# Kernel tuning notes

Measured on AMD Instinct MI355X. Metric: run time of the kernel, lower is better.

## Reference

```python
import jax, jax.numpy as jnp
import numpy as np

C_IN = 128
C_HID = 32
N_HEADS = 4
INF = 1000000000.0


def setup_inputs() -> dict:
    key = jax.random.key(0)
    ks = jax.random.split(key, 12)
    B, I, J = 1, 256, 256
    hc = N_HEADS * C_HID
    s = 0.02
    return {
        "x": jax.random.normal(ks[0], (B, I, J, C_IN), dtype=jnp.float32),
        "mask": jnp.ones((B, I, J), dtype=jnp.float32),
        "ln_w": jnp.ones((C_IN,), dtype=jnp.float32),
        "ln_b": jnp.zeros((C_IN,), dtype=jnp.float32),
        "w_tri": jax.random.normal(ks[1], (C_IN, N_HEADS), dtype=jnp.float32) * s,
        "wq": jax.random.normal(ks[2], (C_IN, hc), dtype=jnp.float32) * s,
        "wk": jax.random.normal(ks[3], (C_IN, hc), dtype=jnp.float32) * s,
        "wv": jax.random.normal(ks[4], (C_IN, hc), dtype=jnp.float32) * s,
        "wg": jax.random.normal(ks[5], (C_IN, hc), dtype=jnp.float32) * s,
        "bg": jnp.ones((hc,), dtype=jnp.float32),
        "wo": jax.random.normal(ks[6], (hc, C_IN), dtype=jnp.float32) * s,
        "bo": jnp.zeros((C_IN,), dtype=jnp.float32),
    }


def _layer_norm(x, w, b, eps=1e-5):
    mu = jnp.mean(x, axis=-1, keepdims=True)
    var = jnp.var(x, axis=-1, keepdims=True)
    return (x - mu) * jax.lax.rsqrt(var + eps) * w + b


def _triangle_attention(x, mask, ln_w, ln_b, w_tri, wq, wk, wv, wg, bg, wo, bo):
    # starting=True: no transpose. x: [B, I, J, C]
    B, I, J, C = x.shape
    x = _layer_norm(x, ln_w, ln_b)
    # mask_bias: [B, I, 1, 1, J]
    mask_bias = (INF * (mask - 1.0))[..., :, None, None, :]
    # triangle_bias: linear(x) -> [B, I, J, H], permute (2,0,1) -> [B, H, I, J], unsqueeze -> [B, 1, H, I, J]
    tri = jnp.einsum("bijc,ch->bhij", x, w_tri)[:, None]  # [B, 1, H, I, J]
    # q/k/v: [B, I, H, J, Ch]
    def proj(w):
        return jnp.einsum("bijc,c(" + "" + ")->bijc", x, w) if False else (
            (x @ w).reshape(B, I, J, N_HEADS, C_HID).transpose(0, 1, 3, 2, 4))
    q = proj(wq) * (C_HID ** -0.5)
    k = proj(wk)
    v = proj(wv)
    # scores: [B, I, H, J, J]; biases broadcast over H (mask_bias) / I (tri over b,1 dim matches i? no)
    scores = jnp.einsum("bihqc,bihkc->bihqk", q, k)
    scores = scores + mask_bias + tri  # tri [B,1,H,I,J] broadcasts: i-dim aligns with query? matches torch broadcast [B,I,H,J,J]+[B,1,H,J,J]... wait tri is [B,1,H,I,J] with I==J so it broadcasts over the batch-of-rows dim
    a = jax.nn.softmax(scores, axis=-1)
    o = jnp.einsum("bihqk,bihkc->bihqc", a, v)  # [B, I, H, J, Ch]
    o = o.transpose(0, 1, 3, 2, 4).reshape(B, I, J, N_HEADS * C_HID)
    g = jax.nn.sigmoid(x @ wg + bg)
    o = o * g
    return o @ wo + bo  # [B, I, J, C]


def reference(x, mask, ln_w, ln_b, w_tri, wq, wk, wv, wg, bg, wo, bo):
    return _triangle_attention(x, mask, ln_w, ln_b, w_tri, wq, wk, wv, wg, bg, wo, bo)
```

## Files before the change

kernel.cpp:

```cpp
#include <hip/hip_runtime.h>


typedef __attribute__((ext_vector_type(4))) float f32x4;
typedef __attribute__((ext_vector_type(8))) short bf16x8;
#define MFMA16(a, b, c) __builtin_amdgcn_mfma_f32_16x16x32_bf16(a, b, c, 0, 0, 0)
#define LOG2E 1.4426950408889634f

__device__ __forceinline__ float bf2f(unsigned int u16) {
    return __uint_as_float(u16 << 16);
}
__device__ __forceinline__ unsigned int f2bf(float f) {
    unsigned int u = __float_as_uint(f);
    return (u + 0x7fffu + ((u >> 16) & 1u)) >> 16;
}
__device__ __forceinline__ unsigned int pack2(float a, float b) {
    return f2bf(a) | (f2bf(b) << 16);
}
__device__ __forceinline__ unsigned int cvt_pk_bf16(float lo, float hi) {
    unsigned int r;
    asm("v_cvt_pk_bf16_f32 %0, %1, %2" : "=v"(r) : "v"(lo), "v"(hi));
    return r;
}

__global__ __launch_bounds__(128) void k_prep(
    const float* __restrict__ wq, const float* __restrict__ wk,
    const float* __restrict__ wv, const float* __restrict__ wg,
    const float* __restrict__ wo, unsigned short* __restrict__ wT)
{
    const int mat = blockIdx.x, k0 = blockIdx.y * 16, t = threadIdx.x;
    const float* W = (mat == 0) ? wq : (mat == 1) ? wk : (mat == 2) ? wv
                     : (mat == 3) ? wg : wo;
    unsigned short* T = wT + mat * 16384;
    float col[16];
    #pragma unroll
    for (int kk = 0; kk < 16; ++kk) col[kk] = W[(k0 + kk) * 128 + t];
    unsigned int pk[8];
    #pragma unroll
    for (int u = 0; u < 8; ++u) pk[u] = pack2(col[2 * u], col[2 * u + 1]);
    *(uint4*)(T + t * 128 + k0)     = make_uint4(pk[0], pk[1], pk[2], pk[3]);
    *(uint4*)(T + t * 128 + k0 + 8) = make_uint4(pk[4], pk[5], pk[6], pk[7]);
}

__global__ __launch_bounds__(256, 2) void k_lnproj(
    const float* __restrict__ x, const float* __restrict__ ln_w,
    const float* __restrict__ ln_b, const float* __restrict__ w_tri,
    const unsigned short* __restrict__ wT, const float* __restrict__ bg,
    unsigned short* __restrict__ qb, unsigned short* __restrict__ kb,
    unsigned short* __restrict__ vtb, unsigned short* __restrict__ gb,
    float* __restrict__ triT)
{
    __shared__ unsigned short sA[128 * 136];
    __shared__ unsigned short sB[128 * 136];
    __shared__ unsigned short sWt[16 * 136];

    const int t = threadIdx.x, w = t >> 6, lane = t & 63;
    const int l15 = lane & 15, g = lane >> 4;
    const int rowBase = blockIdx.x * 128;

    if (t < 128) {
        const float4 wv = ((const float4*)w_tri)[t];
        sWt[0 * 136 + t] = (unsigned short)f2bf(wv.x);
        sWt[1 * 136 + t] = (unsigned short)f2bf(wv.y);
        sWt[2 * 136 + t] = (unsigned short)f2bf(wv.z);
        sWt[3 * 136 + t] = (unsigned short)f2bf(wv.w);
    } else {
        #pragma unroll
        for (int u = 0; u < 13; ++u) {
            const int idx = (t - 128) + 128 * u;
            if (idx < 12 * 136) sWt[4 * 136 + idx] = 0;
        }
    }

    {
        const int r = t >> 1, half = t & 1;
        const float* xr = x + (size_t)(rowBase + r) * 128 + half * 64;
        float v[64];
        float s1 = 0.0f, s2 = 0.0f;
        #pragma unroll
        for (int u = 0; u < 16; ++u) {
            const float4 q4 = ((const float4*)xr)[u];
            v[4*u] = q4.x; v[4*u+1] = q4.y; v[4*u+2] = q4.z; v[4*u+3] = q4.w;
            s1 += q4.x + q4.y + q4.z + q4.w;
            s2 += q4.x*q4.x + q4.y*q4.y + q4.z*q4.z + q4.w*q4.w;
        }
        s1 += __shfl_xor(s1, 1);
        s2 += __shfl_xor(s2, 1);
        const float mu = s1 * (1.0f / 128.0f);
        const float rs = rsqrtf(s2 * (1.0f / 128.0f) - mu * mu + 1e-5f);
        const float4* lw = (const float4*)(ln_w + half * 64);
        const float4* lb = (const float4*)(ln_b + half * 64);
        #pragma unroll
        for (int u = 0; u < 16; ++u) {
            const float4 w4 = lw[u], b4 = lb[u];
            v[4*u]   = (v[4*u]   - mu) * rs * w4.x + b4.x;
            v[4*u+1] = (v[4*u+1] - mu) * rs * w4.y + b4.y;
            v[4*u+2] = (v[4*u+2] - mu) * rs * w4.z + b4.z;
            v[4*u+3] = (v[4*u+3] - mu) * rs * w4.w + b4.w;
        }
        #pragma unroll
        for (int u = 0; u < 8; ++u) {
            uint4 pk;
            pk.x = pack2(v[8*u],   v[8*u+1]);
            pk.y = pack2(v[8*u+2], v[8*u+3]);
            pk.z = pack2(v[8*u+4], v[8*u+5]);
            pk.w = pack2(v[8*u+6], v[8*u+7]);
            *(uint4*)&sA[r * 136 + half * 64 + u * 8] = pk;
        }
    }
    __syncthreads();

    bf16x8 af[2][4];
    #pragma unroll
    for (int m = 0; m < 2; ++m)
        #pragma unroll
        for (int ks = 0; ks < 4; ++ks)
            af[m][ks] = *(const bf16x8*)&sA[(w * 32 + m * 16 + l15) * 136 + ks * 32 + g * 8];

    #pragma unroll
    for (int m = 0; m < 2; ++m) {
        f32x4 tc = (f32x4){0.f, 0.f, 0.f, 0.f};
        #pragma unroll
        for (int ks = 0; ks < 4; ++ks) {
            const bf16x8 bfw = *(const bf16x8*)&sWt[l15 * 136 + ks * 32 + g * 8];
            tc = MFMA16(af[m][ks], bfw, tc);
        }
        if (l15 < 4) {
            #pragma unroll
            for (int reg = 0; reg < 4; ++reg) {
                const int gr = rowBase + w * 32 + m * 16 + 4 * g + reg;
                triT[l15 * 65536 + gr] = tc[reg] * LOG2E;
            }
        }
    }

    const int r2 = t >> 1, half2 = t & 1;
    for (int mat = 0; mat < 4; ++mat) {
        {
            const unsigned short* Wm = wT + mat * 16384 + r2 * 128 + half2 * 64;
            #pragma unroll
            for (int u = 0; u < 8; ++u)
                *(uint4*)&sB[r2 * 136 + half2 * 64 + u * 8] = *(const uint4*)(Wm + u * 8);
        }
        __syncthreads();

        f32x4 acc[2][8];
        #pragma unroll
        for (int m = 0; m < 2; ++m)
            #pragma unroll
            for (int n = 0; n < 8; ++n) acc[m][n] = (f32x4){0.f, 0.f, 0.f, 0.f};
        #pragma unroll
        for (int n = 0; n < 8; ++n)
            #pragma unroll
            for (int ks = 0; ks < 4; ++ks) {
                const bf16x8 bf = *(const bf16x8*)&sB[(n * 16 + l15) * 136 + ks * 32 + g * 8];
                acc[0][n] = MFMA16(af[0][ks], bf, acc[0][n]);
                acc[1][n] = MFMA16(af[1][ks], bf, acc[1][n]);
            }
        __syncthreads();

        float bgv[8];
        if (mat == 3) {
            #pragma unroll
            for (int n = 0; n < 8; ++n) bgv[n] = bg[n * 16 + l15];
        }
        const float scl = (mat == 0) ? 0.25503486245f : 1.0f;
        #pragma unroll
        for (int m = 0; m < 2; ++m)
            #pragma unroll
            for (int n = 0; n < 8; ++n) {
                float vv[4];
                #pragma unroll
                for (int reg = 0; reg < 4; ++reg) {
                    float z = acc[m][n][reg];
                    if (mat == 3) z = 1.0f / (1.0f + __expf(-(z + bgv[n])));
                    else z *= scl;
                    vv[reg] = z;
                }
                const unsigned int a01 = cvt_pk_bf16(vv[0], vv[1]);
                const unsigned int a23 = cvt_pk_bf16(vv[2], vv[3]);
                const int qr = w * 32 + m * 16 + g * 4;
                const int col = n * 16 + l15;
                sB[qr * 136 + col]       = (unsigned short)a01;
                sB[(qr + 1) * 136 + col] = (unsigned short)(a01 >> 16);
                sB[(qr + 2) * 136 + col] = (unsigned short)a23;
                sB[(qr + 3) * 136 + col] = (unsigned short)(a23 >> 16);
            }
        __syncthreads();

        const int row = rowBase + r2;
        if (mat < 2) {
            unsigned short* dst = (mat == 0) ? qb : kb;
            const int i = row >> 8, j = row & 255;
            #pragma unroll
            for (int u = 0; u < 8; ++u) {
                const int c0 = half2 * 64 + u * 8;
                const int hh = c0 >> 5, ch = c0 & 31;
                *(uint4*)(dst + (((size_t)(i * 4 + hh)) * 256 + j) * 32 + ch) =
                    *(const uint4*)&sB[r2 * 136 + c0];
            }
        } else if (mat == 2) {
            const int c = t & 127, jh = t >> 7;
            const int i = rowBase >> 8;
            const int j0 = (rowBase & 255) + jh * 64;
            unsigned short buf[64];
            #pragma unroll
            for (int u = 0; u < 64; ++u) buf[u] = sB[(jh * 64 + u) * 136 + c];
            unsigned short* dst = vtb + ((size_t)(i * 128 + c)) * 256 + j0;
            #pragma unroll
            for (int u = 0; u < 8; ++u)
                *(uint4*)(dst + u * 8) = *(uint4*)&buf[u * 8];
        } else {
            #pragma unroll
            for (int u = 0; u < 8; ++u) {
                const int c0 = half2 * 64 + u * 8;
                *(uint4*)(gb + (size_t)row * 128 + c0) = *(const uint4*)&sB[r2 * 136 + c0];
            }
        }
        __syncthreads();
    }
}

__global__ __launch_bounds__(256, 3) void k_attn5(
    const unsigned short* __restrict__ qb, const unsigned short* __restrict__ kb,
    const unsigned short* __restrict__ vtb, const float* __restrict__ mask,
    const float* __restrict__ triT, unsigned short* __restrict__ ob)
{
    __shared__ unsigned short sK[256 * 36];
    __shared__ unsigned short sP[4][64 * 64];
    __shared__ float sM[256];

    const int i = blockIdx.x, h = blockIdx.y, t = threadIdx.x;
    const int w = t >> 6, lane = t & 63, l15 = lane & 15, g = lane >> 4;
    const size_t base = (size_t)(i * 4 + h) * 8192;

    {
        const uint4* ks = (const uint4*)(kb + base + t * 32);
        uint4 k0 = ks[0], k1 = ks[1], k2 = ks[2], k3 = ks[3];
        *(uint4*)&sK[t * 36]      = k0;
        *(uint4*)&sK[t * 36 + 8]  = k1;
        *(uint4*)&sK[t * 36 + 16] = k2;
        *(uint4*)&sK[t * 36 + 24] = k3;
        sM[t] = (LOG2E * 1.0e9f) * (mask[i * 256 + t] - 1.0f);
    }

    const int q0 = w * 64;
    bf16x8 qf[4];
    #pragma unroll
    for (int m = 0; m < 4; ++m)
        qf[m] = *(const bf16x8*)(qb + base + (size_t)(q0 + m * 16 + l15) * 32 + g * 8);

    bf16x8 ones;
    #pragma unroll
    for (int u = 0; u < 8; ++u) ones[u] = (short)0x3F80;

    __syncthreads();

    f32x4 acc[4][2], accL[4];
    #pragma unroll
    for (int m = 0; m < 4; ++m) {
        acc[m][0] = (f32x4){0.f, 0.f, 0.f, 0.f};
        acc[m][1] = (f32x4){0.f, 0.f, 0.f, 0.f};
        accL[m]   = (f32x4){0.f, 0.f, 0.f, 0.f};
    }

    char* sPw = (char*)&sP[w][0];
    const int swz = (l15 & 7) << 4;
    const float* triQ = triT + h * 65536;
    const f32x4 zero = (f32x4){0.f, 0.f, 0.f, 0.f};

    for (int kt = 0; kt < 4; ++kt) {
        const int kv0 = kt * 64;
        bf16x8 kf[4];
        #pragma unroll
        for (int n = 0; n < 4; ++n)
            kf[n] = *(const bf16x8*)&sK[(kv0 + n * 16 + l15) * 36 + g * 8];

        float4 mk[4];
        #pragma unroll
        for (int n = 0; n < 4; ++n) mk[n] = *(const float4*)&sM[kv0 + n * 16 + g * 4];

        float4 tvb[2][4];
        #pragma unroll
        for (int n = 0; n < 4; ++n)
            tvb[0][n] = *(const float4*)(triQ + (q0 + l15) * 256 + kv0 + n * 16 + g * 4);

        #pragma unroll
        for (int m = 0; m < 4; ++m) {
            f32x4 p[4];
            #pragma unroll
            for (int n = 0; n < 4; ++n)
                p[n] = MFMA16(kf[n], qf[m], zero);
            if (m < 3) {
                #pragma unroll
                for (int n = 0; n < 4; ++n)
                    tvb[(m + 1) & 1][n] = *(const float4*)
                        (triQ + (q0 + (m + 1) * 16 + l15) * 256 + kv0 + n * 16 + g * 4);
            }
            #pragma unroll
            for (int n = 0; n < 4; ++n) {
                const float4 tv = tvb[m & 1][n];
                p[n][0] = exp2f(p[n][0] + mk[n].x + tv.x);
                p[n][1] = exp2f(p[n][1] + mk[n].y + tv.y);
                p[n][2] = exp2f(p[n][2] + mk[n].z + tv.z);
                p[n][3] = exp2f(p[n][3] + mk[n].w + tv.w);
            }
            #pragma unroll
            for (int n = 0; n < 4; ++n) {
                const unsigned int a01 = cvt_pk_bf16(p[n][0], p[n][1]);
                const unsigned int a23 = cvt_pk_bf16(p[n][2], p[n][3]);
                *(uint2*)(sPw + (m * 16 + l15) * 128 + ((n * 32 + g * 8) ^ swz)) =
                    make_uint2(a01, a23);
            }
        }

        #pragma unroll
        for (int ks = 0; ks < 2; ++ks) {
            const bf16x8 vf0 = *(const bf16x8*)
                (vtb + base + (size_t)l15 * 256 + kv0 + ks * 32 + g * 8);
            const bf16x8 vf1 = *(const bf16x8*)
                (vtb + base + (size_t)(16 + l15) * 256 + kv0 + ks * 32 + g * 8);
            #pragma unroll
            for (int m = 0; m < 4; ++m) {
                const bf16x8 pb = *(const bf16x8*)
                    (sPw + (m * 16 + l15) * 128 + ((ks * 64 + g * 16) ^ swz));
                acc[m][0] = MFMA16(vf0, pb, acc[m][0]);
                acc[m][1] = MFMA16(vf1, pb, acc[m][1]);
                accL[m]   = MFMA16(ones, pb, accL[m]);
            }
        }
    }

    #pragma unroll
    for (int m = 0; m < 4; ++m) {
        const float inv = 1.0f / accL[m][0];
        const int q = q0 + m * 16 + l15;
        unsigned short* op = ob + (((size_t)(i * 256 + q)) * 4 + h) * 32;
        #pragma unroll
        for (int n2 = 0; n2 < 2; ++n2) {
            const unsigned int a01 = cvt_pk_bf16(acc[m][n2][0] * inv, acc[m][n2][1] * inv);
            const unsigned int a23 = cvt_pk_bf16(acc[m][n2][2] * inv, acc[m][n2][3] * inv);
            *(uint2*)(op + n2 * 16 + g * 4) = make_uint2(a01, a23);
        }
    }
}

__global__ __launch_bounds__(256, 2) void k_out2(
    const unsigned short* __restrict__ ob, const unsigned short* __restrict__ gb,
    const unsigned short* __restrict__ woT, const float* __restrict__ bo,
    float* __restrict__ out)
{
    __shared__ unsigned short sA[128 * 136];
    __shared__ unsigned short sB[128 * 136];
    const int t = threadIdx.x, w = t >> 6, lane = t & 63;
    const int l15 = lane & 15, g = lane >> 4;
    const int rowBase = blockIdx.x * 128;

    {
        const int r = t >> 1, half = t & 1;
        #pragma unroll
        for (int u = 0; u < 8; ++u) {
            const int c = half * 64 + u * 8;
            const uint4 ov = *(const uint4*)(ob + (size_t)(rowBase + r) * 128 + c);
            const uint4 gv = *(const uint4*)(gb + (size_t)(rowBase + r) * 128 + c);
            uint4 pr;
            pr.x = cvt_pk_bf16(bf2f(ov.x & 0xffffu) * bf2f(gv.x & 0xffffu),
                               bf2f(ov.x >> 16) * bf2f(gv.x >> 16));
            pr.y = cvt_pk_bf16(bf2f(ov.y & 0xffffu) * bf2f(gv.y & 0xffffu),
                               bf2f(ov.y >> 16) * bf2f(gv.y >> 16));
            pr.z = cvt_pk_bf16(bf2f(ov.z & 0xffffu) * bf2f(gv.z & 0xffffu),
                               bf2f(ov.z >> 16) * bf2f(gv.z >> 16));
            pr.w = cvt_pk_bf16(bf2f(ov.w & 0xffffu) * bf2f(gv.w & 0xffffu),
                               bf2f(ov.w >> 16) * bf2f(gv.w >> 16));
            *(uint4*)&sA[r * 136 + c] = pr;
            *(uint4*)&sB[r * 136 + c] = *(const uint4*)(woT + r * 128 + c);
        }
    }
    __syncthreads();

    f32x4 acc[2][8];
    #pragma unroll
    for (int m = 0; m < 2; ++m)
        #pragma unroll
        for (int n = 0; n < 8; ++n) acc[m][n] = (f32x4){0.f, 0.f, 0.f, 0.f};

    bf16x8 af[2][4];
    #pragma unroll
    for (int m = 0; m < 2; ++m)
        #pragma unroll
        for (int ks = 0; ks < 4; ++ks)
            af[m][ks] = *(const bf16x8*)&sA[(w * 32 + m * 16 + l15) * 136 + ks * 32 + g * 8];
    #pragma unroll
    for (int n = 0; n < 8; ++n) {
        #pragma unroll
        for (int ks = 0; ks < 4; ++ks) {
            const bf16x8 bf = *(const bf16x8*)&sB[(n * 16 + l15) * 136 + ks * 32 + g * 8];
            acc[0][n] = MFMA16(af[0][ks], bf, acc[0][n]);
            acc[1][n] = MFMA16(af[1][ks], bf, acc[1][n]);
        }
    }

    float bov[8];
    #pragma unroll
    for (int n = 0; n < 8; ++n) bov[n] = bo[n * 16 + l15];
    #pragma unroll
    for (int m = 0; m < 2; ++m)
        #pragma unroll
        for (int n = 0; n < 8; ++n)
            #pragma unroll
            for (int reg = 0; reg < 4; ++reg) {
                const int row = rowBase + w * 32 + m * 16 + g * 4 + reg;
                out[(size_t)row * 128 + n * 16 + l15] = acc[m][n][reg] + bov[n];
            }
}

extern "C" void kernel_launch(void* const* d_in, const int* in_sizes, int n_in,
                              void* d_out, int out_size, void* d_ws, size_t ws_size,
                              hipStream_t stream) {
    (void)in_sizes; (void)n_in; (void)out_size; (void)ws_size;
    const float* x     = (const float*)d_in[0];
    const float* mask  = (const float*)d_in[1];
    const float* ln_w  = (const float*)d_in[2];
    const float* ln_b  = (const float*)d_in[3];
    const float* w_tri = (const float*)d_in[4];
    const float* wq    = (const float*)d_in[5];
    const float* wk    = (const float*)d_in[6];
    const float* wv    = (const float*)d_in[7];
    const float* wg    = (const float*)d_in[8];
    const float* bg    = (const float*)d_in[9];
    const float* wo    = (const float*)d_in[10];
    const float* bo    = (const float*)d_in[11];
    float* out = (float*)d_out;

    char* ws = (char*)d_ws;
    unsigned short* qb   = (unsigned short*)(ws + (16u << 20));
    unsigned short* kb   = (unsigned short*)(ws + (32u << 20));
    unsigned short* vtb  = (unsigned short*)(ws + (48u << 20));
    unsigned short* gb   = (unsigned short*)(ws + (64u << 20));
    unsigned short* ob   = (unsigned short*)(ws + (80u << 20));
    float*          triT = (float*)(ws + (96u << 20));
    unsigned short* wT   = (unsigned short*)(ws + (97u << 20));

    k_prep<<<dim3(5, 8), 128, 0, stream>>>(wq, wk, wv, wg, wo, wT);
    k_lnproj<<<512, 256, 0, stream>>>(x, ln_w, ln_b, w_tri, wT, bg,
                                      qb, kb, vtb, gb, triT);
    k_attn5<<<dim3(256, 4), 256, 0, stream>>>(qb, kb, vtb, mask, triT, ob);
    k_out2<<<512, 256, 0, stream>>>(ob, gb, wT + 4 * 16384, bo, out);
}
```

Baseline: 123.3 us.

## Fuse gating into attention epilogue, stage V in LDS, shrink out-proj LDS

Moves the sigmoid-gate multiply from the output-projection kernel into the attention kernel epilogue, so the output kernel no longer reads the gate tensor. The attention kernel now stages V^T into shared memory, processes keys in 32-wide halves with a smaller P buffer, and uses an XOR swizzle for K in LDS. The output kernel loads the weight matrix in two K-chunks to cut LDS use and raise occupancy to three blocks per CU. The costs are extra barriers in the output kernel, more LDS in the attention kernel, and an extra gate read per attention block.

```diff
diff --git a/kernel.cpp b/kernel.cpp
--- a/kernel.cpp
+++ b/kernel.cpp
@@ -220,13 +220,15 @@
     }
 }
 
-__global__ __launch_bounds__(256, 3) void k_attn5(
+__global__ __launch_bounds__(256, 3) void k_attn6(
     const unsigned short* __restrict__ qb, const unsigned short* __restrict__ kb,
     const unsigned short* __restrict__ vtb, const float* __restrict__ mask,
-    const float* __restrict__ triT, unsigned short* __restrict__ ob)
+    const float* __restrict__ triT, const unsigned short* __restrict__ gb,
+    unsigned short* __restrict__ ob)
 {
-    __shared__ unsigned short sK[256 * 36];
-    __shared__ unsigned short sP[4][64 * 64];
+    __shared__ unsigned short sK[256 * 32];
+    __shared__ unsigned short sVt[32 * 260];
+    __shared__ unsigned short sP[4][64 * 36];
     __shared__ float sM[256];
 
     const int i = blockIdx.x, h = blockIdx.y, t = threadIdx.x;
@@ -235,11 +237,19 @@
 
     {
         const uint4* ks = (const uint4*)(kb + base + t * 32);
-        uint4 k0 = ks[0], k1 = ks[1], k2 = ks[2], k3 = ks[3];
-        *(uint4*)&sK[t * 36]      = k0;
-        *(uint4*)&sK[t * 36 + 8]  = k1;
-        *(uint4*)&sK[t * 36 + 16] = k2;
-        *(uint4*)&sK[t * 36 + 24] = k3;
+        char* kdst = (char*)sK + t * 64;
+        const int kswz = (t & 3) << 4;
+        #pragma unroll
+        for (int u = 0; u < 4; ++u)
+            *(uint4*)(kdst + ((u * 16) ^ kswz)) = ks[u];
+
+        const int ch = t >> 3, seg = t & 7;
+        const uint4* vs = (const uint4*)(vtb + base + (size_t)ch * 256 + seg * 32);
+        unsigned short* vdst = &sVt[ch * 260 + seg * 32];
+        #pragma unroll
+        for (int u = 0; u < 4; ++u)
+            *(uint4*)(vdst + u * 8) = vs[u];
+
         sM[t] = (LOG2E * 1.0e9f) * (mask[i * 256 + t] - 1.0f);
     }
 
@@ -263,66 +273,69 @@
         accL[m]   = (f32x4){0.f, 0.f, 0.f, 0.f};
     }
 
-    char* sPw = (char*)&sP[w][0];
-    const int swz = (l15 & 7) << 4;
+    unsigned short* sPw = &sP[w][0];
     const float* triQ = triT + h * 65536;
     const f32x4 zero = (f32x4){0.f, 0.f, 0.f, 0.f};
 
+    #pragma unroll
     for (int kt = 0; kt < 4; ++kt) {
         const int kv0 = kt * 64;
-        bf16x8 kf[4];
-        #pragma unroll
-        for (int n = 0; n < 4; ++n)
-            kf[n] = *(const bf16x8*)&sK[(kv0 + n * 16 + l15) * 36 + g * 8];
-
-        float4 mk[4];
-        #pragma unroll
-        for (int n = 0; n < 4; ++n) mk[n] = *(const float4*)&sM[kv0 + n * 16 + g * 4];
-
-        float4 tvb[2][4];
-        #pragma unroll
-        for (int n = 0; n < 4; ++n)
-            tvb[0][n] = *(const float4*)(triQ + (q0 + l15) * 256 + kv0 + n * 16 + g * 4);
-
-        #pragma unroll
-        for (int m = 0; m < 4; ++m) {
-            f32x4 p[4];
-            #pragma unroll
-            for (int n = 0; n < 4; ++n)
-                p[n] = MFMA16(kf[n], qf[m], zero);
-            if (m < 3) {
+        #pragma unroll
+        for (int hh = 0; hh < 2; ++hh) {
+            const int kvh = kv0 + hh * 32;
+
+            bf16x8 kf[2];
+            #pragma unroll
+            for (int n2 = 0; n2 < 2; ++n2) {
+                const int row = kvh + n2 * 16 + l15;
+                kf[n2] = *(const bf16x8*)((const char*)sK + row * 64 +
+                                          ((g * 16) ^ ((row & 3) << 4)));
+            }
+            float4 mk[2];
+            #pragma unroll
+            for (int n2 = 0; n2 < 2; ++n2)
+                mk[n2] = *(const float4*)&sM[kvh + n2 * 16 + g * 4];
+
+            float4 tvb[2][2];
+            #pragma unroll
+            for (int n2 = 0; n2 < 2; ++n2)
+                tvb[0][n2] = *(const float4*)
+                    (triQ + (q0 + l15) * 256 + kvh + n2 * 16 + g * 4);
+
+            #pragma unroll
+            for (int m = 0; m < 4; ++m) {
+                f32x4 p[2];
                 #pragma unroll
-                for (int n = 0; n < 4; ++n)
-                    tvb[(m + 1) & 1][n] = *(const float4*)
-                        (triQ + (q0 + (m + 1) * 16 + l15) * 256 + kv0 + n * 16 + g * 4);
-            }
-            #pragma unroll
-            for (int n = 0; n < 4; ++n) {
-                const float4 tv = tvb[m & 1][n];
-                p[n][0] = exp2f(p[n][0] + mk[n].x + tv.x);
-                p[n][1] = exp2f(p[n][1] + mk[n].y + tv.y);
-                p[n][2] = exp2f(p[n][2] + mk[n].z + tv.z);
-                p[n][3] = exp2f(p[n][3] + mk[n].w + tv.w);
-            }
-            #pragma unroll
-            for (int n = 0; n < 4; ++n) {
-                const unsigned int a01 = cvt_pk_bf16(p[n][0], p[n][1]);
-                const unsigned int a23 = cvt_pk_bf16(p[n][2], p[n][3]);
-                *(uint2*)(sPw + (m * 16 + l15) * 128 + ((n * 32 + g * 8) ^ swz)) =
-                    make_uint2(a01, a23);
-            }
-        }
-
-        #pragma unroll
-        for (int ks = 0; ks < 2; ++ks) {
-            const bf16x8 vf0 = *(const bf16x8*)
-                (vtb + base + (size_t)l15 * 256 + kv0 + ks * 32 + g * 8);
-            const bf16x8 vf1 = *(const bf16x8*)
-                (vtb + base + (size_t)(16 + l15) * 256 + kv0 + ks * 32 + g * 8);
+                for (int n2 = 0; n2 < 2; ++n2)
+                    p[n2] = MFMA16(kf[n2], qf[m], zero);
+                if (m < 3) {
+                    #pragma unroll
+                    for (int n2 = 0; n2 < 2; ++n2)
+                        tvb[(m + 1) & 1][n2] = *(const float4*)
+                            (triQ + (q0 + (m + 1) * 16 + l15) * 256 + kvh + n2 * 16 + g * 4);
+                }
+                #pragma unroll
+                for (int n2 = 0; n2 < 2; ++n2) {
+                    const float4 tv = tvb[m & 1][n2];
+                    p[n2][0] = exp2f(p[n2][0] + mk[n2].x + tv.x);
+                    p[n2][1] = exp2f(p[n2][1] + mk[n2].y + tv.y);
+                    p[n2][2] = exp2f(p[n2][2] + mk[n2].z + tv.z);
+                    p[n2][3] = exp2f(p[n2][3] + mk[n2].w + tv.w);
+                }
+                #pragma unroll
+                for (int n2 = 0; n2 < 2; ++n2) {
+                    const unsigned int a01 = cvt_pk_bf16(p[n2][0], p[n2][1]);
+                    const unsigned int a23 = cvt_pk_bf16(p[n2][2], p[n2][3]);
+                    *(uint2*)&sPw[(m * 16 + l15) * 36 + n2 * 16 + g * 4] =
+                        make_uint2(a01, a23);
+                }
+            }
+
+            const bf16x8 vf0 = *(const bf16x8*)&sVt[l15 * 260 + kvh + g * 8];
+            const bf16x8 vf1 = *(const bf16x8*)&sVt[(16 + l15) * 260 + kvh + g * 8];
             #pragma unroll
             for (int m = 0; m < 4; ++m) {
-                const bf16x8 pb = *(const bf16x8*)
-                    (sPw + (m * 16 + l15) * 128 + ((ks * 64 + g * 16) ^ swz));
+                const bf16x8 pb = *(const bf16x8*)&sPw[(m * 16 + l15) * 36 + g * 8];
                 acc[m][0] = MFMA16(vf0, pb, acc[m][0]);
                 acc[m][1] = MFMA16(vf1, pb, acc[m][1]);
                 accL[m]   = MFMA16(ones, pb, accL[m]);
@@ -334,48 +347,38 @@
     for (int m = 0; m < 4; ++m) {
         const float inv = 1.0f / accL[m][0];
         const int q = q0 + m * 16 + l15;
+        const unsigned short* gp = gb + (size_t)(i * 256 + q) * 128 + h * 32;
         unsigned short* op = ob + (((size_t)(i * 256 + q)) * 4 + h) * 32;
         #pragma unroll
         for (int n2 = 0; n2 < 2; ++n2) {
-            const unsigned int a01 = cvt_pk_bf16(acc[m][n2][0] * inv, acc[m][n2][1] * inv);
-            const unsigned int a23 = cvt_pk_bf16(acc[m][n2][2] * inv, acc[m][n2][3] * inv);
+            const uint2 gv = *(const uint2*)(gp + n2 * 16 + g * 4);
+            const float g0 = bf2f(gv.x & 0xffffu), g1 = bf2f(gv.x >> 16);
+            const float g2 = bf2f(gv.y & 0xffffu), g3 = bf2f(gv.y >> 16);
+            const unsigned int a01 =
+                cvt_pk_bf16(acc[m][n2][0] * inv * g0, acc[m][n2][1] * inv * g1);
+            const unsigned int a23 =
+                cvt_pk_bf16(acc[m][n2][2] * inv * g2, acc[m][n2][3] * inv * g3);
             *(uint2*)(op + n2 * 16 + g * 4) = make_uint2(a01, a23);
         }
     }
 }
 
-__global__ __launch_bounds__(256, 2) void k_out2(
-    const unsigned short* __restrict__ ob, const unsigned short* __restrict__ gb,
-    const unsigned short* __restrict__ woT, const float* __restrict__ bo,
-    float* __restrict__ out)
+__global__ __launch_bounds__(256, 3) void k_out3(
+    const unsigned short* __restrict__ ob, const unsigned short* __restrict__ woT,
+    const float* __restrict__ bo, float* __restrict__ out)
 {
     __shared__ unsigned short sA[128 * 136];
-    __shared__ unsigned short sB[128 * 136];
+    __shared__ unsigned short sB[128 * 72];
     const int t = threadIdx.x, w = t >> 6, lane = t & 63;
     const int l15 = lane & 15, g = lane >> 4;
     const int rowBase = blockIdx.x * 128;
-
-    {
-        const int r = t >> 1, half = t & 1;
-        #pragma unroll
-        for (int u = 0; u < 8; ++u) {
-            const int c = half * 64 + u * 8;
-            const uint4 ov = *(const uint4*)(ob + (size_t)(rowBase + r) * 128 + c);
-            const uint4 gv = *(const uint4*)(gb + (size_t)(rowBase + r) * 128 + c);
-            uint4 pr;
-            pr.x = cvt_pk_bf16(bf2f(ov.x & 0xffffu) * bf2f(gv.x & 0xffffu),
-                               bf2f(ov.x >> 16) * bf2f(gv.x >> 16));
-            pr.y = cvt_pk_bf16(bf2f(ov.y & 0xffffu) * bf2f(gv.y & 0xffffu),
-                               bf2f(ov.y >> 16) * bf2f(gv.y >> 16));
-            pr.z = cvt_pk_bf16(bf2f(ov.z & 0xffffu) * bf2f(gv.z & 0xffffu),
-                               bf2f(ov.z >> 16) * bf2f(gv.z >> 16));
-            pr.w = cvt_pk_bf16(bf2f(ov.w & 0xffffu) * bf2f(gv.w & 0xffffu),
-                               bf2f(ov.w >> 16) * bf2f(gv.w >> 16));
-            *(uint4*)&sA[r * 136 + c] = pr;
-            *(uint4*)&sB[r * 136 + c] = *(const uint4*)(woT + r * 128 + c);
-        }
-    }
-    __syncthreads();
+    const int r = t >> 1, half = t & 1;
+
+    #pragma unroll
+    for (int u = 0; u < 8; ++u) {
+        const int c = half * 64 + u * 8;
+        *(uint4*)&sA[r * 136 + c] = *(const uint4*)(ob + (size_t)(rowBase + r) * 128 + c);
+    }
 
     f32x4 acc[2][8];
     #pragma unroll
@@ -383,20 +386,27 @@
         #pragma unroll
         for (int n = 0; n < 8; ++n) acc[m][n] = (f32x4){0.f, 0.f, 0.f, 0.f};
 
-    bf16x8 af[2][4];
-    #pragma unroll
-    for (int m = 0; m < 2; ++m)
-        #pragma unroll
-        for (int ks = 0; ks < 4; ++ks)
-            af[m][ks] = *(const bf16x8*)&sA[(w * 32 + m * 16 + l15) * 136 + ks * 32 + g * 8];
-    #pragma unroll
-    for (int n = 0; n < 8; ++n) {
-        #pragma unroll
-        for (int ks = 0; ks < 4; ++ks) {
-            const bf16x8 bf = *(const bf16x8*)&sB[(n * 16 + l15) * 136 + ks * 32 + g * 8];
-            acc[0][n] = MFMA16(af[0][ks], bf, acc[0][n]);
-            acc[1][n] = MFMA16(af[1][ks], bf, acc[1][n]);
-        }
+    #pragma unroll
+    for (int kc = 0; kc < 2; ++kc) {
+        #pragma unroll
+        for (int u = 0; u < 4; ++u)
+            *(uint4*)&sB[r * 72 + half * 32 + u * 8] =
+                *(const uint4*)(woT + r * 128 + kc * 64 + half * 32 + u * 8);
+        __syncthreads();
+        #pragma unroll
+        for (int ks = 0; ks < 2; ++ks) {
+            const bf16x8 a0 = *(const bf16x8*)
+                &sA[(w * 32 + l15) * 136 + kc * 64 + ks * 32 + g * 8];
+            const bf16x8 a1 = *(const bf16x8*)
+                &sA[(w * 32 + 16 + l15) * 136 + kc * 64 + ks * 32 + g * 8];
+            #pragma unroll
+            for (int n = 0; n < 8; ++n) {
+                const bf16x8 bf = *(const bf16x8*)&sB[(n * 16 + l15) * 72 + ks * 32 + g * 8];
+                acc[0][n] = MFMA16(a0, bf, acc[0][n]);
+                acc[1][n] = MFMA16(a1, bf, acc[1][n]);
+            }
+        }
+        __syncthreads();
     }
 
     float bov[8];
@@ -443,6 +453,6 @@
     k_prep<<<dim3(5, 8), 128, 0, stream>>>(wq, wk, wv, wg, wo, wT);
     k_lnproj<<<512, 256, 0, stream>>>(x, ln_w, ln_b, w_tri, wT, bg,
                                       qb, kb, vtb, gb, triT);
-    k_attn5<<<dim3(256, 4), 256, 0, stream>>>(qb, kb, vtb, mask, triT, ob);
-    k_out2<<<512, 256, 0, stream>>>(ob, gb, wT + 4 * 16384, bo, out);
-}
+    k_attn6<<<dim3(256, 4), 256, 0, stream>>>(qb, kb, vtb, mask, triT, gb, ob);
+    k_out3<<<512, 256, 0, stream>>>(ob, wT + 4 * 16384, bo, out);
+}
```

Result: faster. 106.3 us (-13.8%).
